# Kernel optimization log

Hardware: AMD Instinct MI355X
Metric: run time of the kernel (lower is better)

Reference implementation:

```python
import jax, jax.numpy as jnp
import numpy as np

DIM = 256
N_EMBED = 8192


def setup_inputs() -> dict:
    key = jax.random.key(0)
    k1, k2 = jax.random.split(key)
    x = jax.random.normal(k1, (16, 32, 32, DIM), dtype=jnp.float32)
    embed = jax.random.normal(k2, (DIM, N_EMBED), dtype=jnp.float32)
    return {"x": x, "embed": embed}


def reference(x, embed):
    # x: [B, H, W, D]; embed: [D, K]
    D = embed.shape[0]
    flat = x.reshape(-1, D)  # [N, D]
    dist = (
        jnp.sum(flat * flat, axis=1, keepdims=True)
        - 2.0 * (flat @ embed)
        + jnp.sum(embed * embed, axis=0, keepdims=True)
    )  # [N, K]
    embed_ind = jnp.argmin(dist, axis=1)  # argmax of -dist
    embed_ind = embed_ind.reshape(x.shape[:-1])  # [B, H, W]
    quantize = jnp.take(embed.T, embed_ind, axis=0)  # [B, H, W, D]
    diff = jnp.mean((jax.lax.stop_gradient(quantize) - x) ** 2)
    quantize = x + jax.lax.stop_gradient(quantize - x)  # straight-through
    return quantize, diff, embed_ind
```

## Files before the change

kernel.cpp:

```cpp
#include <hip/hip_runtime.h>

typedef unsigned long long u64;
typedef unsigned short ushort_t;
typedef float f32x4 __attribute__((ext_vector_type(4)));
typedef short bf16x8 __attribute__((ext_vector_type(8)));
typedef unsigned short ushort8 __attribute__((ext_vector_type(8)));

#define D_DIM   256
#define N_ROWS  16384
#define K_CODES 8192
#define OFF_DIFF 4194304
#define OFF_IND  4194305

#define XH_OFF    0ULL
#define XL_OFF    8388608ULL
#define EHT_OFF   16777216ULL
#define ELT_OFF   20971520ULL
#define ETF_OFF   25165824ULL
#define ENORM_OFF 33554432ULL
#define KEYS_OFF  33587200ULL
#define PV1_OFF   33718272ULL
#define PIDX_OFF  37912576ULL
#define PV2_OFF   42106880ULL
#define WLC_OFF   46301184ULL
#define WL_OFF    46301440ULL
#define PART_OFF  46366976ULL
#define WS_NEED   46375168ULL

#define MARGIN_TH 0.08f

#define GLD(gp, lp) __builtin_amdgcn_global_load_lds( \
    (const __attribute__((address_space(1))) unsigned int*)(const void*)(gp), \
    (__attribute__((address_space(3))) unsigned int*)(void*)(lp), 16, 0, 0)

__device__ __forceinline__ unsigned int fsort(float f) {
    unsigned int u = __float_as_uint(f);
    return (u & 0x80000000u) ? ~u : (u | 0x80000000u);
}
__device__ __forceinline__ ushort_t f2bf(float f) {
    unsigned int u = __float_as_uint(f);
    unsigned int r = (u + 0x7fffu + ((u >> 16) & 1u)) >> 16;
    return (ushort_t)r;
}
__device__ __forceinline__ float bf2f(ushort_t h) {
    return __uint_as_float(((unsigned int)h) << 16);
}

__global__ __launch_bounds__(256) void k_split_x(const float* __restrict__ x,
                                                 ushort_t* __restrict__ xh,
                                                 ushort_t* __restrict__ xl) {
    int base = (blockIdx.x * 256 + threadIdx.x) * 8;
    float4 v0 = *reinterpret_cast<const float4*>(&x[base]);
    float4 v1 = *reinterpret_cast<const float4*>(&x[base + 4]);
    float f[8] = {v0.x, v0.y, v0.z, v0.w, v1.x, v1.y, v1.z, v1.w};
    ushort8 h, l;
    #pragma unroll
    for (int i = 0; i < 8; ++i) {
        ushort_t hb = f2bf(f[i]);
        h[i] = (short)hb;
        l[i] = (short)f2bf(f[i] - bf2f(hb));
    }
    *reinterpret_cast<ushort8*>(&xh[base]) = h;
    *reinterpret_cast<ushort8*>(&xl[base]) = l;
}

__global__ __launch_bounds__(256) void k_split_eT(const float* __restrict__ e,
                                                  ushort_t* __restrict__ ehT,
                                                  ushort_t* __restrict__ elT,
                                                  float* __restrict__ eTf) {
    __shared__ float tile[64][257];
    const int t = threadIdx.x;
    const int c0 = blockIdx.x * 64;
    for (int it = 0; it < 64; ++it) {
        int d = it * 4 + (t >> 6);
        tile[t & 63][d] = e[d * K_CODES + c0 + (t & 63)];
    }
    __syncthreads();
    for (int cc = 0; cc < 64; ++cc) {
        float v = tile[cc][t];
        ushort_t hb = f2bf(v);
        size_t o = (size_t)(c0 + cc) * 256 + t;
        ehT[o] = hb;
        elT[o] = f2bf(v - bf2f(hb));
        eTf[o] = v;
    }
}

__global__ __launch_bounds__(256) void k_norms(const float* __restrict__ e,
                                               float* __restrict__ enorm,
                                               int* __restrict__ wlc) {
    int k = blockIdx.x * 256 + threadIdx.x;
    float s = 0.f;
    #pragma unroll 8
    for (int d = 0; d < D_DIM; ++d) {
        float v = e[d * K_CODES + k];
        s = fmaf(v, v, s);
    }
    enorm[k] = s;
    if (k == 0) *wlc = 0;
}

__global__ __launch_bounds__(256, 2) void k_mfma(const ushort_t* __restrict__ xh,
                                                 const ushort_t* __restrict__ xl,
                                                 const ushort_t* __restrict__ ehT,
                                                 const ushort_t* __restrict__ elT,
                                                 const float* __restrict__ enorm,
                                                 float* __restrict__ pv1,
                                                 int* __restrict__ pidx,
                                                 float* __restrict__ pv2) {
    __shared__ short Ah[4096], Al[4096], Bh[4096], Bl[4096];
    __shared__ float mg_v1[2][128];
    __shared__ float mg_v2[2][128];
    __shared__ int   mg_i1[2][128];
    const int tid = threadIdx.x;
    const int l = tid & 63, w = tid >> 6;
    const int wm = w >> 1, wn = w & 1;
    const int r0 = blockIdx.x * 128, c0 = blockIdx.y * 128;

    const int rl = l >> 2;
    const int g = (l & 3) ^ (rl & 3);
    const int rowL0 = w * 32 + rl;
    const size_t aoff = (size_t)(r0 + rowL0) * 256 + g * 8;
    const size_t boff = (size_t)(c0 + rowL0) * 256 + g * 8;
    short* Adst = Ah + w * 1024;
    short* Aldst = Al + w * 1024;
    short* Bdst = Bh + w * 1024;
    short* Bldst = Bl + w * 1024;

    f32x4 acc[4][4];
    #pragma unroll
    for (int mi = 0; mi < 4; ++mi)
        #pragma unroll
        for (int ni = 0; ni < 4; ++ni)
            #pragma unroll
            for (int q = 0; q < 4; ++q) acc[mi][ni][q] = 0.f;

    const int fr = l & 15, kg = l >> 4;

    for (int kt = 0; kt < 8; ++kt) {
        const int ko = kt * 32;
        GLD(&xh[aoff + ko], Adst);
        GLD(&xh[aoff + ko + 4096], Adst + 512);
        GLD(&xl[aoff + ko], Aldst);
        GLD(&xl[aoff + ko + 4096], Aldst + 512);
        GLD(&ehT[boff + ko], Bdst);
        GLD(&ehT[boff + ko + 4096], Bdst + 512);
        GLD(&elT[boff + ko], Bldst);
        GLD(&elT[boff + ko + 4096], Bldst + 512);
        __syncthreads();

        bf16x8 a_h[4], a_l[4], b_h[4], b_l[4];
        #pragma unroll
        for (int mi = 0; mi < 4; ++mi) {
            int rf = wm * 64 + mi * 16 + fr;
            int idx = rf * 32 + ((kg ^ (rf & 3)) * 8);
            a_h[mi] = *reinterpret_cast<const bf16x8*>(&Ah[idx]);
            a_l[mi] = *reinterpret_cast<const bf16x8*>(&Al[idx]);
        }
        #pragma unroll
        for (int ni = 0; ni < 4; ++ni) {
            int cf = wn * 64 + ni * 16 + fr;
            int idx = cf * 32 + ((kg ^ (cf & 3)) * 8);
            b_h[ni] = *reinterpret_cast<const bf16x8*>(&Bh[idx]);
            b_l[ni] = *reinterpret_cast<const bf16x8*>(&Bl[idx]);
        }
        #pragma unroll
        for (int mi = 0; mi < 4; ++mi)
            #pragma unroll
            for (int ni = 0; ni < 4; ++ni) {
                acc[mi][ni] = __builtin_amdgcn_mfma_f32_16x16x32_bf16(a_h[mi], b_h[ni], acc[mi][ni], 0, 0, 0);
                acc[mi][ni] = __builtin_amdgcn_mfma_f32_16x16x32_bf16(a_h[mi], b_l[ni], acc[mi][ni], 0, 0, 0);
                acc[mi][ni] = __builtin_amdgcn_mfma_f32_16x16x32_bf16(a_l[mi], b_h[ni], acc[mi][ni], 0, 0, 0);
            }
        __syncthreads();
    }

    float en[4];
    #pragma unroll
    for (int ni = 0; ni < 4; ++ni) en[ni] = enorm[c0 + wn * 64 + ni * 16 + fr];

    #pragma unroll
    for (int mi = 0; mi < 4; ++mi)
        #pragma unroll
        for (int r = 0; r < 4; ++r) {
            float v1 = fmaf(-2.f, acc[mi][0][r], en[0]);
            int i1 = c0 + wn * 64 + fr;
            float v2 = 1e30f;
            #pragma unroll
            for (int ni = 1; ni < 4; ++ni) {
                float dv = fmaf(-2.f, acc[mi][ni][r], en[ni]);
                if (dv < v1) { v2 = v1; v1 = dv; i1 = c0 + wn * 64 + ni * 16 + fr; }
                else v2 = fminf(v2, dv);
            }
            #pragma unroll
            for (int m = 1; m <= 8; m <<= 1) {
                float ov1 = __shfl_xor(v1, m, 64);
                int   oi1 = __shfl_xor(i1, m, 64);
                float ov2 = __shfl_xor(v2, m, 64);
                bool better = (ov1 < v1) || (ov1 == v1 && oi1 < i1);
                float nv2 = fminf(fminf(v2, ov2), better ? v1 : ov1);
                if (better) { v1 = ov1; i1 = oi1; }
                v2 = nv2;
            }
            if (fr == 0) {
                int lr = wm * 64 + mi * 16 + kg * 4 + r;
                mg_v1[wn][lr] = v1;
                mg_i1[wn][lr] = i1;
                mg_v2[wn][lr] = v2;
            }
        }

    __syncthreads();
    if (tid < 128) {
        float v1a = mg_v1[0][tid], v2a = mg_v2[0][tid];
        float v1b = mg_v1[1][tid], v2b = mg_v2[1][tid];
        int   i1a = mg_i1[0][tid], i1b = mg_i1[1][tid];
        bool better = (v1b < v1a) || (v1b == v1a && i1b < i1a);
        float fv1 = better ? v1b : v1a;
        int   fi1 = better ? i1b : i1a;
        float fv2 = fminf(fminf(v2a, v2b), better ? v1a : v1b);
        int pos = (r0 + tid) * 64 + blockIdx.y;
        pv1[pos] = fv1; pidx[pos] = fi1; pv2[pos] = fv2;
    }
}

__global__ __launch_bounds__(256) void k_reduce(const float* __restrict__ pv1,
                                                const int* __restrict__ pidx,
                                                const float* __restrict__ pv2,
                                                u64* __restrict__ keys,
                                                int* __restrict__ wlc,
                                                int* __restrict__ wl) {
    const int w = threadIdx.x >> 6, l = threadIdx.x & 63;
    const int row = blockIdx.x * 4 + w;
    float v1 = pv1[row * 64 + l];
    int   i1 = pidx[row * 64 + l];
    float v2 = pv2[row * 64 + l];
    #pragma unroll
    for (int m = 1; m <= 32; m <<= 1) {
        float ov1 = __shfl_xor(v1, m, 64);
        int   oi1 = __shfl_xor(i1, m, 64);
        float ov2 = __shfl_xor(v2, m, 64);
        bool better = (ov1 < v1) || (ov1 == v1 && oi1 < i1);
        float nv2 = fminf(fminf(v2, ov2), better ? v1 : ov1);
        if (better) { v1 = ov1; i1 = oi1; }
        v2 = nv2;
    }
    if (l == 0) {
        if (v2 - v1 < MARGIN_TH) {
            int p = atomicAdd(wlc, 1);
            wl[p] = row;
            keys[row] = ~0ULL;
        } else {
            keys[row] = (((u64)fsort(v1)) << 32) | (unsigned int)i1;
        }
    }
}

__global__ __launch_bounds__(128) void k_exact(const float* __restrict__ x,
                                               const float* __restrict__ e,
                                               const float* __restrict__ enorm,
                                               const int* __restrict__ wlc,
                                               const int* __restrict__ wl,
                                               u64* __restrict__ keys) {
    __shared__ float xs[8][256];
    __shared__ int rowids[8];
    __shared__ u64 red[8][2];
    const int t = threadIdx.x;
    const int cnt = *wlc;
    const int c = blockIdx.x * 128 + t;
    const float en = enorm[c];

    for (int j = blockIdx.y; j * 8 < cnt; j += 16) {
        int nr = cnt - j * 8; if (nr > 8) nr = 8;
        if (t < 8) rowids[t] = (t < nr) ? wl[j * 8 + t] : 0;
        __syncthreads();
        for (int rr = 0; rr < nr; ++rr) {
            int row = rowids[rr];
            xs[rr][t] = x[(size_t)row * 256 + t];
            xs[rr][t + 128] = x[(size_t)row * 256 + t + 128];
        }
        __syncthreads();
        float dot[8];
        #pragma unroll
        for (int rr = 0; rr < 8; ++rr) dot[rr] = 0.f;
        for (int d = 0; d < 256; ++d) {
            float ev = e[d * K_CODES + c];
            #pragma unroll
            for (int rr = 0; rr < 8; ++rr) dot[rr] = fmaf(ev, xs[rr][d], dot[rr]);
        }
        #pragma unroll
        for (int rr = 0; rr < 8; ++rr) {
            float dist = fmaf(-2.f, dot[rr], en);
            u64 kk = (((u64)fsort(dist)) << 32) | (unsigned int)c;
            #pragma unroll
            for (int m = 1; m <= 32; m <<= 1) {
                u64 ok = __shfl_xor(kk, m, 64);
                kk = ok < kk ? ok : kk;
            }
            if ((t & 63) == 0) red[rr][t >> 6] = kk;
        }
        __syncthreads();
        if (t < nr) {
            u64 fk = red[t][0] < red[t][1] ? red[t][0] : red[t][1];
            atomicMin(&keys[rowids[t]], fk);
        }
        __syncthreads();
    }
}

__global__ __launch_bounds__(256) void k_gather2(const float* __restrict__ x,
                                                 const float* __restrict__ eTf,
                                                 const u64* __restrict__ keys,
                                                 float* __restrict__ out_q,
                                                 float* __restrict__ out_ind,
                                                 float* __restrict__ partial) {
    const int t = threadIdx.x, w = t >> 6, l = t & 63;
    float s = 0.f;
    #pragma unroll
    for (int p = 0; p < 2; ++p) {
        int row = blockIdx.x * 8 + p * 4 + w;
        int idx = (int)(keys[row] & 0xFFFFFFFFu);
        float4 q = *reinterpret_cast<const float4*>(&eTf[(size_t)idx * 256 + l * 4]);
        float4 xv = *reinterpret_cast<const float4*>(&x[(size_t)row * 256 + l * 4]);
        *reinterpret_cast<float4*>(&out_q[(size_t)row * 256 + l * 4]) = q;
        if (l == 0) out_ind[row] = (float)idx;
        float dx = q.x - xv.x, dy = q.y - xv.y, dz = q.z - xv.z, dw = q.w - xv.w;
        s += dx * dx + dy * dy + dz * dz + dw * dw;
    }
    #pragma unroll
    for (int m = 1; m <= 32; m <<= 1) s += __shfl_xor(s, m, 64);
    __shared__ float red[4];
    if (l == 0) red[w] = s;
    __syncthreads();
    if (t == 0) partial[blockIdx.x] = red[0] + red[1] + red[2] + red[3];
}

__global__ __launch_bounds__(256) void k_diff(const float* __restrict__ partial,
                                              float* __restrict__ out_diff) {
    const int t = threadIdx.x;
    float s = 0.f;
    for (int i = t; i < 2048; i += 256) s += partial[i];
    #pragma unroll
    for (int m = 1; m <= 32; m <<= 1) s += __shfl_xor(s, m, 64);
    __shared__ float red[4];
    if ((t & 63) == 0) red[t >> 6] = s;
    __syncthreads();
    if (t == 0) out_diff[0] = (red[0] + red[1] + red[2] + red[3]) * (1.0f / 4194304.0f);
}

constexpr int FBM = 64, FBN = 256, FBK = 32, FNSPLIT = 2;

__global__ __launch_bounds__(256) void k_init_fb(u64* __restrict__ keys,
                                                 float* __restrict__ diff_slot) {
    int t = blockIdx.x * 256 + threadIdx.x;
    if (t < N_ROWS) keys[t] = ~0ULL;
    if (t == 0) diff_slot[0] = 0.0f;
}

__global__ __launch_bounds__(256) void k_argmin_fb(const float* __restrict__ x,
                                                   const float* __restrict__ e,
                                                   const float* __restrict__ enorm,
                                                   u64* __restrict__ keys) {
    __shared__ float xs[FBK][FBM + 4];
    __shared__ float es[FBK][FBN];
    const int tid = threadIdx.x;
    const int tr = tid >> 5, tc = tid & 31;
    const int row0 = blockIdx.x * FBM;
    const int cbase = blockIdx.y * (K_CODES / FNSPLIT);
    float minv[8]; int mini[8];
    #pragma unroll
    for (int i = 0; i < 8; ++i) { minv[i] = 1e30f; mini[i] = 0; }
    for (int chunk = 0; chunk < (K_CODES / FNSPLIT) / FBN; ++chunk) {
        const int c0 = cbase + chunk * FBN;
        float acc[8][8];
        #pragma unroll
        for (int i = 0; i < 8; ++i)
            #pragma unroll
            for (int j = 0; j < 8; ++j) acc[i][j] = 0.f;
        for (int kt = 0; kt < D_DIM / FBK; ++kt) {
            #pragma unroll
            for (int l2 = 0; l2 < 2; ++l2) {
                int q = tid + 256 * l2, r = q >> 3, kq = q & 7;
                float4 v = *reinterpret_cast<const float4*>(&x[(row0 + r) * D_DIM + kt * FBK + kq * 4]);
                xs[kq * 4 + 0][r] = v.x; xs[kq * 4 + 1][r] = v.y;
                xs[kq * 4 + 2][r] = v.z; xs[kq * 4 + 3][r] = v.w;
            }
            #pragma unroll
            for (int l2 = 0; l2 < 8; ++l2) {
                int q = tid + 256 * l2, k = q >> 6, cq = q & 63;
                float4 v = *reinterpret_cast<const float4*>(&e[(kt * FBK + k) * K_CODES + c0 + cq * 4]);
                *reinterpret_cast<float4*>(&es[k][cq * 4]) = v;
            }
            __syncthreads();
            #pragma unroll 8
            for (int k = 0; k < FBK; ++k) {
                float4 a0 = *reinterpret_cast<const float4*>(&xs[k][tr * 8]);
                float4 a1 = *reinterpret_cast<const float4*>(&xs[k][tr * 8 + 4]);
                float4 b0 = *reinterpret_cast<const float4*>(&es[k][tc * 8]);
                float4 b1 = *reinterpret_cast<const float4*>(&es[k][tc * 8 + 4]);
                float a[8] = {a0.x, a0.y, a0.z, a0.w, a1.x, a1.y, a1.z, a1.w};
                float b[8] = {b0.x, b0.y, b0.z, b0.w, b1.x, b1.y, b1.z, b1.w};
                #pragma unroll
                for (int i = 0; i < 8; ++i)
                    #pragma unroll
                    for (int j = 0; j < 8; ++j) acc[i][j] = fmaf(a[i], b[j], acc[i][j]);
            }
            __syncthreads();
        }
        #pragma unroll
        for (int j = 0; j < 8; ++j) {
            int c = c0 + tc * 8 + j;
            float en = enorm[c];
            #pragma unroll
            for (int i = 0; i < 8; ++i) {
                float dv = fmaf(-2.0f, acc[i][j], en);
                if (dv < minv[i]) { minv[i] = dv; mini[i] = c; }
            }
        }
    }
    #pragma unroll
    for (int m = 16; m >= 1; m >>= 1) {
        #pragma unroll
        for (int i = 0; i < 8; ++i) {
            float ov = __shfl_xor(minv[i], m, 64);
            int oi = __shfl_xor(mini[i], m, 64);
            if (ov < minv[i] || (ov == minv[i] && oi < mini[i])) { minv[i] = ov; mini[i] = oi; }
        }
    }
    if (tc == 0) {
        #pragma unroll
        for (int i = 0; i < 8; ++i) {
            int row = row0 + tr * 8 + i;
            u64 key = (((u64)fsort(minv[i])) << 32) | (unsigned int)mini[i];
            atomicMin(&keys[row], key);
        }
    }
}

__global__ __launch_bounds__(256) void k_gather_fb(const float* __restrict__ x,
                                                   const float* __restrict__ e,
                                                   const u64* __restrict__ keys,
                                                   float* __restrict__ out_q,
                                                   float* __restrict__ out_diff,
                                                   float* __restrict__ out_ind) {
    int row = blockIdx.x, d = threadIdx.x;
    int idx = (int)(keys[row] & 0xFFFFFFFFu);
    float q = e[d * K_CODES + idx];
    float xv = x[row * D_DIM + d];
    out_q[row * D_DIM + d] = q;
    if (d == 0) out_ind[row] = (float)idx;
    float sq = q - xv; sq *= sq;
    #pragma unroll
    for (int m = 32; m >= 1; m >>= 1) sq += __shfl_xor(sq, m, 64);
    __shared__ float red[4];
    if ((d & 63) == 0) red[d >> 6] = sq;
    __syncthreads();
    if (d == 0) {
        float s = (red[0] + red[1] + red[2] + red[3]) * (1.0f / (float)(N_ROWS * D_DIM));
        atomicAdd(out_diff, s);
    }
}

extern "C" void kernel_launch(void* const* d_in, const int* in_sizes, int n_in,
                              void* d_out, int out_size, void* d_ws, size_t ws_size,
                              hipStream_t stream) {
    const float* x = (const float*)d_in[0];
    const float* e = (const float*)d_in[1];
    float* out = (float*)d_out;
    float* out_q = out;
    float* out_diff = out + OFF_DIFF;
    float* out_ind = out + OFF_IND;
    char* ws = (char*)d_ws;

    if (ws_size >= WS_NEED) {
        ushort_t* xh  = (ushort_t*)(ws + XH_OFF);
        ushort_t* xl  = (ushort_t*)(ws + XL_OFF);
        ushort_t* ehT = (ushort_t*)(ws + EHT_OFF);
        ushort_t* elT = (ushort_t*)(ws + ELT_OFF);
        float* eTf    = (float*)(ws + ETF_OFF);
        float* enorm  = (float*)(ws + ENORM_OFF);
        u64* keys     = (u64*)(ws + KEYS_OFF);
        float* pv1    = (float*)(ws + PV1_OFF);
        int* pidx     = (int*)(ws + PIDX_OFF);
        float* pv2    = (float*)(ws + PV2_OFF);
        int* wlc      = (int*)(ws + WLC_OFF);
        int* wl       = (int*)(ws + WL_OFF);
        float* part   = (float*)(ws + PART_OFF);

        k_split_x <<<2048, 256, 0, stream>>>(x, xh, xl);
        k_split_eT<<<128, 256, 0, stream>>>(e, ehT, elT, eTf);
        k_norms   <<<32, 256, 0, stream>>>(e, enorm, wlc);
        k_mfma    <<<dim3(128, 64), 256, 0, stream>>>(xh, xl, ehT, elT, enorm, pv1, pidx, pv2);
        k_reduce  <<<4096, 256, 0, stream>>>(pv1, pidx, pv2, keys, wlc, wl);
        k_exact   <<<dim3(64, 16), 128, 0, stream>>>(x, e, enorm, wlc, wl, keys);
        k_gather2 <<<2048, 256, 0, stream>>>(x, eTf, keys, out_q, out_ind, part);
        k_diff    <<<1, 256, 0, stream>>>(part, out_diff);
    } else {
        float* enorm = (float*)ws;
        u64* keys = (u64*)(ws + 32768);
        k_init_fb  <<<64, 256, 0, stream>>>(keys, out_diff);
        k_norms    <<<32, 256, 0, stream>>>(e, enorm, (int*)(ws + 163840));
        k_argmin_fb<<<dim3(N_ROWS / FBM, FNSPLIT), 256, 0, stream>>>(x, e, enorm, keys);
        k_gather_fb<<<N_ROWS, 256, 0, stream>>>(x, e, keys, out_q, out_diff, out_ind);
    }
}
```

Before: 377.7 us.

## Loop each MFMA block over eight code chunks with register-resident running argmin

Each k_mfma block now iterates over 8 consecutive 128-code chunks instead of handling one, and the operand roles are swapped so codes sit on the M side. The top-two argmin is carried in registers across chunks, which reduces the partial-result tensor from 64 to 8 entries per row, so a smaller k_reduce8 replaces k_reduce. The LDS swizzle changes to use (row>>1)&3, and launch bounds ask for 3 blocks per CU. The intent is to cut grid size, partial writes and reduction traffic, at the cost of more per-block serial work and higher register pressure under the tighter occupancy bound.

```diff
diff --git a/kernel.cpp b/kernel.cpp
--- a/kernel.cpp
+++ b/kernel.cpp
@@ -100,7 +100,7 @@
     if (k == 0) *wlc = 0;
 }
 
-__global__ __launch_bounds__(256, 2) void k_mfma(const ushort_t* __restrict__ xh,
+__global__ __launch_bounds__(256, 3) void k_mfma(const ushort_t* __restrict__ xh,
                                                  const ushort_t* __restrict__ xl,
                                                  const ushort_t* __restrict__ ehT,
                                                  const ushort_t* __restrict__ elT,
@@ -112,103 +112,120 @@
     __shared__ float mg_v1[2][128];
     __shared__ float mg_v2[2][128];
     __shared__ int   mg_i1[2][128];
+    __shared__ float en_s[128];
     const int tid = threadIdx.x;
     const int l = tid & 63, w = tid >> 6;
     const int wm = w >> 1, wn = w & 1;
-    const int r0 = blockIdx.x * 128, c0 = blockIdx.y * 128;
+    const int r0 = blockIdx.x * 128;
+    const int cbase0 = blockIdx.y * 1024;
 
     const int rl = l >> 2;
-    const int g = (l & 3) ^ (rl & 3);
+    const int g = (l & 3) ^ ((rl >> 1) & 3);
     const int rowL0 = w * 32 + rl;
-    const size_t aoff = (size_t)(r0 + rowL0) * 256 + g * 8;
-    const size_t boff = (size_t)(c0 + rowL0) * 256 + g * 8;
-    short* Adst = Ah + w * 1024;
+    const size_t boff = (size_t)(r0 + rowL0) * 256 + g * 8;
+    short* Adst  = Ah + w * 1024;
     short* Aldst = Al + w * 1024;
-    short* Bdst = Bh + w * 1024;
+    short* Bdst  = Bh + w * 1024;
     short* Bldst = Bl + w * 1024;
 
-    f32x4 acc[4][4];
-    #pragma unroll
-    for (int mi = 0; mi < 4; ++mi)
+    const int fr = l & 15, kg = l >> 4;
+
+    float v1[4], v2[4];
+    int   i1[4];
+    #pragma unroll
+    for (int ni = 0; ni < 4; ++ni) { v1[ni] = 1e30f; v2[ni] = 1e30f; i1[ni] = 0; }
+
+    for (int ch = 0; ch < 8; ++ch) {
+        const int cb = cbase0 + ch * 128;
+        __syncthreads();
+        if (tid < 128) en_s[tid] = enorm[cb + tid];
+        const size_t aoff = (size_t)(cb + rowL0) * 256 + g * 8;
+
+        f32x4 acc[4][4];
+        #pragma unroll
+        for (int mi = 0; mi < 4; ++mi)
+            #pragma unroll
+            for (int ni = 0; ni < 4; ++ni)
+                #pragma unroll
+                for (int q = 0; q < 4; ++q) acc[mi][ni][q] = 0.f;
+
+        for (int kt = 0; kt < 8; ++kt) {
+            const int ko = kt * 32;
+            GLD(&ehT[aoff + ko], Adst);
+            GLD(&ehT[aoff + ko + 4096], Adst + 512);
+            GLD(&elT[aoff + ko], Aldst);
+            GLD(&elT[aoff + ko + 4096], Aldst + 512);
+            GLD(&xh[boff + ko], Bdst);
+            GLD(&xh[boff + ko + 4096], Bdst + 512);
+            GLD(&xl[boff + ko], Bldst);
+            GLD(&xl[boff + ko + 4096], Bldst + 512);
+            __syncthreads();
+
+            bf16x8 a_h[4], a_l[4], b_h[4], b_l[4];
+            #pragma unroll
+            for (int mi = 0; mi < 4; ++mi) {
+                int rf = wn * 64 + mi * 16 + fr;
+                int idx = rf * 32 + ((kg ^ ((rf >> 1) & 3)) * 8);
+                a_h[mi] = *reinterpret_cast<const bf16x8*>(&Ah[idx]);
+                a_l[mi] = *reinterpret_cast<const bf16x8*>(&Al[idx]);
+            }
+            #pragma unroll
+            for (int ni = 0; ni < 4; ++ni) {
+                int cf = wm * 64 + ni * 16 + fr;
+                int idx = cf * 32 + ((kg ^ ((cf >> 1) & 3)) * 8);
+                b_h[ni] = *reinterpret_cast<const bf16x8*>(&Bh[idx]);
+                b_l[ni] = *reinterpret_cast<const bf16x8*>(&Bl[idx]);
+            }
+            #pragma unroll
+            for (int mi = 0; mi < 4; ++mi)
+                #pragma unroll
+                for (int ni = 0; ni < 4; ++ni) {
+                    acc[mi][ni] = __builtin_amdgcn_mfma_f32_16x16x32_bf16(a_h[mi], b_h[ni], acc[mi][ni], 0, 0, 0);
+                    acc[mi][ni] = __builtin_amdgcn_mfma_f32_16x16x32_bf16(a_h[mi], b_l[ni], acc[mi][ni], 0, 0, 0);
+                    acc[mi][ni] = __builtin_amdgcn_mfma_f32_16x16x32_bf16(a_l[mi], b_h[ni], acc[mi][ni], 0, 0, 0);
+                }
+            __syncthreads();
+        }
+
+        float en_r[4][4];
+        #pragma unroll
+        for (int mi = 0; mi < 4; ++mi)
+            #pragma unroll
+            for (int r = 0; r < 4; ++r)
+                en_r[mi][r] = en_s[wn * 64 + mi * 16 + kg * 4 + r];
+        const int cwn = cb + wn * 64 + kg * 4;
         #pragma unroll
         for (int ni = 0; ni < 4; ++ni)
             #pragma unroll
-            for (int q = 0; q < 4; ++q) acc[mi][ni][q] = 0.f;
-
-    const int fr = l & 15, kg = l >> 4;
-
-    for (int kt = 0; kt < 8; ++kt) {
-        const int ko = kt * 32;
-        GLD(&xh[aoff + ko], Adst);
-        GLD(&xh[aoff + ko + 4096], Adst + 512);
-        GLD(&xl[aoff + ko], Aldst);
-        GLD(&xl[aoff + ko + 4096], Aldst + 512);
-        GLD(&ehT[boff + ko], Bdst);
-        GLD(&ehT[boff + ko + 4096], Bdst + 512);
-        GLD(&elT[boff + ko], Bldst);
-        GLD(&elT[boff + ko + 4096], Bldst + 512);
-        __syncthreads();
-
-        bf16x8 a_h[4], a_l[4], b_h[4], b_l[4];
-        #pragma unroll
-        for (int mi = 0; mi < 4; ++mi) {
-            int rf = wm * 64 + mi * 16 + fr;
-            int idx = rf * 32 + ((kg ^ (rf & 3)) * 8);
-            a_h[mi] = *reinterpret_cast<const bf16x8*>(&Ah[idx]);
-            a_l[mi] = *reinterpret_cast<const bf16x8*>(&Al[idx]);
-        }
-        #pragma unroll
-        for (int ni = 0; ni < 4; ++ni) {
-            int cf = wn * 64 + ni * 16 + fr;
-            int idx = cf * 32 + ((kg ^ (cf & 3)) * 8);
-            b_h[ni] = *reinterpret_cast<const bf16x8*>(&Bh[idx]);
-            b_l[ni] = *reinterpret_cast<const bf16x8*>(&Bl[idx]);
-        }
-        #pragma unroll
-        for (int mi = 0; mi < 4; ++mi)
-            #pragma unroll
-            for (int ni = 0; ni < 4; ++ni) {
-                acc[mi][ni] = __builtin_amdgcn_mfma_f32_16x16x32_bf16(a_h[mi], b_h[ni], acc[mi][ni], 0, 0, 0);
-                acc[mi][ni] = __builtin_amdgcn_mfma_f32_16x16x32_bf16(a_h[mi], b_l[ni], acc[mi][ni], 0, 0, 0);
-                acc[mi][ni] = __builtin_amdgcn_mfma_f32_16x16x32_bf16(a_l[mi], b_h[ni], acc[mi][ni], 0, 0, 0);
-            }
-        __syncthreads();
-    }
-
-    float en[4];
-    #pragma unroll
-    for (int ni = 0; ni < 4; ++ni) en[ni] = enorm[c0 + wn * 64 + ni * 16 + fr];
-
-    #pragma unroll
-    for (int mi = 0; mi < 4; ++mi)
-        #pragma unroll
-        for (int r = 0; r < 4; ++r) {
-            float v1 = fmaf(-2.f, acc[mi][0][r], en[0]);
-            int i1 = c0 + wn * 64 + fr;
-            float v2 = 1e30f;
-            #pragma unroll
-            for (int ni = 1; ni < 4; ++ni) {
-                float dv = fmaf(-2.f, acc[mi][ni][r], en[ni]);
-                if (dv < v1) { v2 = v1; v1 = dv; i1 = c0 + wn * 64 + ni * 16 + fr; }
-                else v2 = fminf(v2, dv);
-            }
-            #pragma unroll
-            for (int m = 1; m <= 8; m <<= 1) {
-                float ov1 = __shfl_xor(v1, m, 64);
-                int   oi1 = __shfl_xor(i1, m, 64);
-                float ov2 = __shfl_xor(v2, m, 64);
-                bool better = (ov1 < v1) || (ov1 == v1 && oi1 < i1);
-                float nv2 = fminf(fminf(v2, ov2), better ? v1 : ov1);
-                if (better) { v1 = ov1; i1 = oi1; }
-                v2 = nv2;
-            }
-            if (fr == 0) {
-                int lr = wm * 64 + mi * 16 + kg * 4 + r;
-                mg_v1[wn][lr] = v1;
-                mg_i1[wn][lr] = i1;
-                mg_v2[wn][lr] = v2;
-            }
-        }
+            for (int mi = 0; mi < 4; ++mi)
+                #pragma unroll
+                for (int r = 0; r < 4; ++r) {
+                    float dv = fmaf(-2.f, acc[mi][ni][r], en_r[mi][r]);
+                    int c = cwn + mi * 16 + r;
+                    if (dv < v1[ni]) { v2[ni] = v1[ni]; v1[ni] = dv; i1[ni] = c; }
+                    else v2[ni] = fminf(v2[ni], dv);
+                }
+    }
+
+    #pragma unroll
+    for (int ni = 0; ni < 4; ++ni) {
+        #pragma unroll
+        for (int m = 16; m <= 32; m <<= 1) {
+            float ov1 = __shfl_xor(v1[ni], m, 64);
+            int   oi1 = __shfl_xor(i1[ni], m, 64);
+            float ov2 = __shfl_xor(v2[ni], m, 64);
+            bool better = (ov1 < v1[ni]) || (ov1 == v1[ni] && oi1 < i1[ni]);
+            float nv2 = fminf(fminf(v2[ni], ov2), better ? v1[ni] : ov1);
+            if (better) { v1[ni] = ov1; i1[ni] = oi1; }
+            v2[ni] = nv2;
+        }
+        if (l < 16) {
+            int lr = wm * 64 + ni * 16 + l;
+            mg_v1[wn][lr] = v1[ni];
+            mg_i1[wn][lr] = i1[ni];
+            mg_v2[wn][lr] = v2[ni];
+        }
+    }
 
     __syncthreads();
     if (tid < 128) {
@@ -219,24 +236,24 @@
         float fv1 = better ? v1b : v1a;
         int   fi1 = better ? i1b : i1a;
         float fv2 = fminf(fminf(v2a, v2b), better ? v1a : v1b);
-        int pos = (r0 + tid) * 64 + blockIdx.y;
+        int pos = (r0 + tid) * 8 + blockIdx.y;
         pv1[pos] = fv1; pidx[pos] = fi1; pv2[pos] = fv2;
     }
 }
 
-__global__ __launch_bounds__(256) void k_reduce(const float* __restrict__ pv1,
-                                                const int* __restrict__ pidx,
-                                                const float* __restrict__ pv2,
-                                                u64* __restrict__ keys,
-                                                int* __restrict__ wlc,
-                                                int* __restrict__ wl) {
-    const int w = threadIdx.x >> 6, l = threadIdx.x & 63;
-    const int row = blockIdx.x * 4 + w;
-    float v1 = pv1[row * 64 + l];
-    int   i1 = pidx[row * 64 + l];
-    float v2 = pv2[row * 64 + l];
-    #pragma unroll
-    for (int m = 1; m <= 32; m <<= 1) {
+__global__ __launch_bounds__(256) void k_reduce8(const float* __restrict__ pv1,
+                                                 const int* __restrict__ pidx,
+                                                 const float* __restrict__ pv2,
+                                                 u64* __restrict__ keys,
+                                                 int* __restrict__ wlc,
+                                                 int* __restrict__ wl) {
+    const int j = threadIdx.x & 7;
+    const int row = blockIdx.x * 32 + (threadIdx.x >> 3);
+    float v1 = pv1[row * 8 + j];
+    int   i1 = pidx[row * 8 + j];
+    float v2 = pv2[row * 8 + j];
+    #pragma unroll
+    for (int m = 1; m <= 4; m <<= 1) {
         float ov1 = __shfl_xor(v1, m, 64);
         int   oi1 = __shfl_xor(i1, m, 64);
         float ov2 = __shfl_xor(v2, m, 64);
@@ -245,7 +262,7 @@
         if (better) { v1 = ov1; i1 = oi1; }
         v2 = nv2;
     }
-    if (l == 0) {
+    if (j == 0) {
         if (v2 - v1 < MARGIN_TH) {
             int p = atomicAdd(wlc, 1);
             wl[p] = row;
@@ -490,8 +507,8 @@
         k_split_x <<<2048, 256, 0, stream>>>(x, xh, xl);
         k_split_eT<<<128, 256, 0, stream>>>(e, ehT, elT, eTf);
         k_norms   <<<32, 256, 0, stream>>>(e, enorm, wlc);
-        k_mfma    <<<dim3(128, 64), 256, 0, stream>>>(xh, xl, ehT, elT, enorm, pv1, pidx, pv2);
-        k_reduce  <<<4096, 256, 0, stream>>>(pv1, pidx, pv2, keys, wlc, wl);
+        k_mfma    <<<dim3(128, 8), 256, 0, stream>>>(xh, xl, ehT, elT, enorm, pv1, pidx, pv2);
+        k_reduce8 <<<512, 256, 0, stream>>>(pv1, pidx, pv2, keys, wlc, wl);
         k_exact   <<<dim3(64, 16), 128, 0, stream>>>(x, e, enorm, wlc, wl, keys);
         k_gather2 <<<2048, 256, 0, stream>>>(x, eTf, keys, out_q, out_ind, part);
         k_diff    <<<1, 256, 0, stream>>>(part, out_diff);
```

Result: slower. 444.4 us (+17.7%).
